# Optimization experiments

Hardware: AMD Instinct MI355X
Metric: run time of the kernel (lower is better)

Reference implementation:

```python
import jax, jax.numpy as jnp
import numpy as np
import math

N = 4096      # nodes
E = 131072    # edges
D = 256       # hidden / out_features
DIN = 16      # distance_map feature dim
H = 2         # attention heads
HD = D // H   # head dim = 128


def setup_inputs() -> dict:
    key = jax.random.key(0)
    ks = jax.random.split(key, 20)
    s = 0.02
    return {
        "input": jax.random.normal(ks[0], (N, D), jnp.float32),
        "adj": jax.random.randint(ks[1], (2, E), 0, N, jnp.int64),
        "h0": jax.random.normal(ks[2], (N, D), jnp.float32),
        "lamda": 1,
        "alpha": jax.random.uniform(ks[3], (1,), jnp.float32),
        "l": 1,
        "distance_map": jax.random.normal(ks[4], (E, DIN), jnp.float32),
        "norm": jax.random.uniform(ks[5], (E,), jnp.float32),
        # GraphConvolution params
        "weight_local": jax.random.normal(ks[6], (2 * D, D), jnp.float32) * s,
        "weight_global": jax.random.normal(ks[7], (2 * D, D), jnp.float32) * s,
        # EA_GCN.lin : Linear(16, D)
        "lin_w": jax.random.normal(ks[8], (D, DIN), jnp.float32) * s,
        "lin_b": jnp.zeros((D,), jnp.float32),
        # EA_GCN.W_EV : 3D -> 2D -> D -> 16 (GELU between)
        "w1": jax.random.normal(ks[9], (2 * D, 3 * D), jnp.float32) * s,
        "b1": jnp.zeros((2 * D,), jnp.float32),
        "w2": jax.random.normal(ks[10], (D, 2 * D), jnp.float32) * s,
        "b2": jnp.zeros((D,), jnp.float32),
        "w3": jax.random.normal(ks[11], (DIN, D), jnp.float32) * s,
        "b3": jnp.zeros((DIN,), jnp.float32),
        # MultiheadAttention params (torch layout: in_proj [3D, D])
        "in_proj_w": jax.random.normal(ks[12], (3 * D, D), jnp.float32) * s,
        "in_proj_b": jnp.zeros((3 * D,), jnp.float32),
        "out_proj_w": jax.random.normal(ks[13], (D, D), jnp.float32) * s,
        "out_proj_b": jnp.zeros((D,), jnp.float32),
    }


def _mha(x, wi, bi, wo, bo):
    # torch MHA, unbatched (N, D) input, eval mode (dropout off)
    qkv = x @ wi.T + bi                      # [N, 3D]
    q, k, v = jnp.split(qkv, 3, axis=-1)
    q = q.reshape(N, H, HD).transpose(1, 0, 2)  # [H, N, HD]
    k = k.reshape(N, H, HD).transpose(1, 0, 2)
    v = v.reshape(N, H, HD).transpose(1, 0, 2)
    scores = jnp.einsum("hnd,hmd->hnm", q, k) / math.sqrt(HD)
    attn = jax.nn.softmax(scores, axis=-1)
    o = jnp.einsum("hnm,hmd->hnd", attn, v)     # [H, N, HD]
    o = o.transpose(1, 0, 2).reshape(N, D)
    return o @ wo.T + bo


def _ea_gcn(x, edge_index, norm, distance_map, lin_w, lin_b, w1, b1, w2, b2, w3, b3):
    src, dst = edge_index[0], edge_index[1]
    edge_attr = distance_map @ lin_w.T + lin_b               # [E, D]
    msg = norm[:, None] * (x[src] + edge_attr)               # gather + combine
    agg = jax.ops.segment_sum(msg, dst, num_segments=N)      # scatter-add
    x_out = agg + x
    h = jnp.concatenate([x_out[src], edge_attr, x_out[dst]], axis=-1)  # [E, 3D]
    h = jax.nn.gelu(h @ w1.T + b1, approximate=False)
    h = jax.nn.gelu(h @ w2.T + b2, approximate=False)
    dm_out = h @ w3.T + b3                                   # [E, 16]
    return x_out, dm_out


def reference(input, adj, h0, lamda, alpha, l, distance_map, norm,
              weight_local, weight_global, lin_w, lin_b,
              w1, b1, w2, b2, w3, b3,
              in_proj_w, in_proj_b, out_proj_w, out_proj_b):
    theta = min(1.0, math.log(lamda / l + 1.0))
    a = alpha[0]
    h_local, dm_out = _ea_gcn(input, adj, norm, distance_map,
                              lin_w, lin_b, w1, b1, w2, b2, w3, b3)
    h_global = _mha(input, in_proj_w, in_proj_b, out_proj_w, out_proj_b)
    support_local = jnp.concatenate([h_local, h0], axis=1)   # [N, 2D]
    r_local = (1.0 - a) * h_local + a * h0
    support_global = jnp.concatenate([h_global, h0], axis=1)
    r_global = (1.0 - a) * h_global + a * h0
    output_local = theta * (support_local @ weight_local) + (1.0 - theta) * r_local
    output_global = theta * (support_global @ weight_global) + (1.0 - theta) * r_global
    output = output_local + output_global                    # residual=False
    return (output, dm_out)
```

## Files before the change

### kernel.cpp

```cpp
#include <hip/hip_runtime.h>
#include <hip/hip_bf16.h>
#include <math.h>

constexpr int N_   = 4096;
constexpr int E_   = 131072;
constexpr int D_   = 256;
constexpr int DIN_ = 16;
constexpr int D3_  = 768;
constexpr int HD_  = 128;

typedef __bf16 bf16_8 __attribute__((ext_vector_type(8)));
typedef float  f32x4  __attribute__((ext_vector_type(4)));
typedef float  f32x4v __attribute__((ext_vector_type(4)));
typedef unsigned int u32x4 __attribute__((ext_vector_type(4)));

__device__ __forceinline__ unsigned short f2b(float f) {
  unsigned int u = __float_as_uint(f);
  u = u + 0x7fffu + ((u >> 16) & 1u);
  return (unsigned short)(u >> 16);
}
__device__ __forceinline__ float b2f(unsigned short s) {
  return __uint_as_float(((unsigned int)s) << 16);
}
__device__ __forceinline__ unsigned int pack2(unsigned short lo, unsigned short hi) {
// ... 444 lines not shown
  for (int m = 0; m < 2; ++m)
#pragma unroll
    for (int n = 0; n < 8; ++n) {
      int col = j0 + n * 16 + r16;
      float bb = opb[col];
#pragma unroll
      for (int rg = 0; rg < 4; ++rg) {
        int row = m0 + wv * 32 + m * 16 + quad * 4 + rg;
        float v = acc[m][n][rg] + bb;
        size_t idx = (size_t)row * D_ + col;
        hgl[idx] = v;
        hgb[idx] = f2b(v);
      }
    }
}

__global__ __launch_bounds__(256) void k_final_mfma(
    const unsigned short* __restrict__ xbp, const unsigned short* __restrict__ h0b,
    const unsigned short* __restrict__ hgb,
    const unsigned short* __restrict__ wlT, const unsigned short* __restrict__ wgT,
    const float* __restrict__ hl, const float* __restrict__ hg, const float* __restrict__ h0,
    const float* __restrict__ alpha_p, const void* lamda_p, const void* l_p,
    float* __restrict__ out) {
  __shared__ unsigned short sA[128][72];
  __shared__ unsigned short sB[128][72];
  const int b   = blockIdx.x;
  const int j0  = (b & 1) * 128;
  const int m0  = (b >> 1) * 128;
  const int tid = threadIdx.x;
  const int lane = tid & 63, wv = tid >> 6;
  const int r16  = lane & 15, quad = lane >> 4;
  const int sr   = tid >> 1, sh = (tid & 1) * 32;

  const f32x4 zz = {0.f, 0.f, 0.f, 0.f};
  f32x4 acc[2][8];
#pragma unroll
  for (int m = 0; m < 2; ++m)
#pragma unroll
    for (int n = 0; n < 8; ++n) acc[m][n] = zz;

  const size_t arow = (size_t)(m0 + sr) * D_;
  const size_t brow = (size_t)(j0 + sr) * 512;

  for (int ki = 0; ki < 16; ++ki) {
    __syncthreads();
    {
      const int gc = ki * 64 + sh;
      const unsigned short* ap =
          (gc < 256) ? xbp + arow + gc
        : (gc < 512) ? h0b + arow + (gc - 256)
        : (gc < 768) ? hgb + arow + (gc - 512)
                     : h0b + arow + (gc - 768);
      const unsigned short* bp = (gc < 512) ? wlT + brow + gc : wgT + brow + (gc - 512);
      const uint4* s    = (const uint4*)ap;
      const uint4* bsrc = (const uint4*)bp;
      uint4* da = (uint4*)&sA[sr][sh];
      uint4* db = (uint4*)&sB[sr][sh];
#pragma unroll
      for (int i = 0; i < 4; ++i) { da[i] = s[i]; db[i] = bsrc[i]; }
    }
    __syncthreads();
#pragma unroll
    for (int kk = 0; kk < 2; ++kk) {
      bf16_8 a0 = frag16(&sA[wv * 32 + r16][kk * 32 + quad * 8]);
      bf16_8 a1 = frag16(&sA[wv * 32 + 16 + r16][kk * 32 + quad * 8]);
#pragma unroll
      for (int n = 0; n < 8; ++n) {
        bf16_8 bf = frag16(&sB[n * 16 + r16][kk * 32 + quad * 8]);
        acc[0][n] = __builtin_amdgcn_mfma_f32_16x16x32_bf16(a0, bf, acc[0][n], 0, 0, 0);
        acc[1][n] = __builtin_amdgcn_mfma_f32_16x16x32_bf16(a1, bf, acc[1][n], 0, 0, 0);
      }
    }
  }
  float theta = fminf(1.f, logf(scalar_as_float(lamda_p) / scalar_as_float(l_p) + 1.f));
  float a = alpha_p[0];
  float omt = 1.f - theta;
#pragma unroll
  for (int m = 0; m < 2; ++m)
#pragma unroll
    for (int n = 0; n < 8; ++n) {
      int col = j0 + n * 16 + r16;
#pragma unroll
      for (int rg = 0; rg < 4; ++rg) {
        int row = m0 + wv * 32 + m * 16 + quad * 4 + rg;
        size_t idx = (size_t)row * D_ + col;
        out[idx] = theta * acc[m][n][rg] +
                   omt * ((1.f - a) * (hl[idx] + hg[idx]) + 2.f * a * h0[idx]);
      }
    }
}

__global__ void k_qk2b(const float* __restrict__ qkv,
                       unsigned short* __restrict__ Qb, unsigned short* __restrict__ Kb) {
  int off = (blockIdx.x * 256 + threadIdx.x) * 8;
  int n = off >> 9, c = off & 511;
  const float* src = qkv + (size_t)n * D3_ + c;
  float4 a = *(const float4*)src;
  float4 b = *(const float4*)(src + 4);
  uint4 p = {pack2(f2b(a.x), f2b(a.y)), pack2(f2b(a.z), f2b(a.w)),
             pack2(f2b(b.x), f2b(b.y)), pack2(f2b(b.z), f2b(b.w))};
  int cc = c & 255;
  int hh = cc >> 7, d = cc & 127;
  unsigned short* dst = (c < 256 ? Qb : Kb) + (size_t)hh * N_ * HD_ + (size_t)n * HD_ + d;
  *(uint4*)dst = p;
}

__global__ __launch_bounds__(256) void k_v2t(const float* __restrict__ qkv,
                                             unsigned short* __restrict__ Vt) {
  __shared__ unsigned short sv[64][136];
  int h = blockIdx.y;
  int n0 = blockIdx.x * 64;
  int tid = threadIdx.x;
#pragma unroll
  for (int it = 0; it < 4; ++it) {
    int off = (tid + it * 256) * 8;
    int r = off >> 7, d = off & 127;
    const float* src = qkv + (size_t)(n0 + r) * D3_ + 2 * D_ + h * HD_ + d;
    float4 a = *(const float4*)src;
    float4 b = *(const float4*)(src + 4);
    uint4 p = {pack2(f2b(a.x), f2b(a.y)), pack2(f2b(a.z), f2b(a.w)),
               pack2(f2b(b.x), f2b(b.y)), pack2(f2b(b.z), f2b(b.w))};
    *(uint4*)&sv[r][d] = p;
  }
  __syncthreads();
#pragma unroll
  for (int it = 0; it < 4; ++it) {
    int off = (tid + it * 256) * 8;
    int d = off >> 6, k = off & 63;
    unsigned short t[8];
#pragma unroll
    for (int j = 0; j < 8; ++j) t[j] = sv[k + j][d];
    uint4 p = {pack2(t[0], t[1]), pack2(t[2], t[3]),
               pack2(t[4], t[5]), pack2(t[6], t[7])};
    *(uint4*)(Vt + (size_t)h * HD_ * N_ + (size_t)d * N_ + n0 + k) = p;
  }
}

__global__ __launch_bounds__(256) void k_attn_mfma(
    const unsigned short* __restrict__ Qb, const unsigned short* __restrict__ Kb,
    const unsigned short* __restrict__ Vt, float* __restrict__ o_out,
    unsigned short* __restrict__ ob) {
  __shared__ unsigned short sK[64][136];
  __shared__ unsigned short sV[128][72];
  __shared__ float          sS[16][68];
  __shared__ unsigned short sP[16][72];
  __shared__ float sm[16], sl[16], sa[16];

  const int tid  = threadIdx.x;
  const int h    = blockIdx.y;
  const int q0   = blockIdx.x * 16;
  const int lane = tid & 63;
  const int wv   = tid >> 6;
  const int r16  = lane & 15;
  const int quad = lane >> 4;

  bf16_8 qf[4];
#pragma unroll
  for (int kk = 0; kk < 4; ++kk)
    qf[kk] = frag16(Qb + (size_t)h * N_ * HD_ + (size_t)(q0 + r16) * HD_ + kk * 32 + quad * 8);

  if (tid < 16) { sm[tid] = -1e30f; sl[tid] = 0.f; }

  const f32x4 zz = {0.f, 0.f, 0.f, 0.f};
  f32x4 o0 = zz, o1 = zz;

  const unsigned short* Kh = Kb + (size_t)h * N_ * HD_;
  const unsigned short* Vh = Vt + (size_t)h * HD_ * N_;

  for (int c0 = 0; c0 < N_; c0 += 64) {
    __syncthreads();
#pragma unroll
    for (int it = 0; it < 4; ++it) {
      int off = (tid + it * 256) * 8;
      int key = off >> 7, d = off & 127;
      *(uint4*)&sK[key][d] = *(const uint4*)(Kh + (size_t)(c0 + key) * HD_ + d);
    }
#pragma unroll
    for (int it = 0; it < 4; ++it) {
      int off = (tid + it * 256) * 8;
      int d = off >> 6, k = off & 63;
      *(uint4*)&sV[d][k] = *(const uint4*)(Vh + (size_t)d * N_ + c0 + k);
    }
    __syncthreads();
    f32x4 s = zz;
#pragma unroll
    for (int kk = 0; kk < 4; ++kk) {
      bf16_8 bf = frag16(&sK[wv * 16 + r16][kk * 32 + quad * 8]);
      s = __builtin_amdgcn_mfma_f32_16x16x32_bf16(qf[kk], bf, s, 0, 0, 0);
    }
    const float sc = 0.08838834764831845f;
#pragma unroll
    for (int r = 0; r < 4; ++r)
      sS[quad * 4 + r][wv * 16 + r16] = s[r] * sc;
    __syncthreads();
    {
      int row = tid >> 4, i = tid & 15;
      float4 v = *(const float4*)&sS[row][i * 4];
      float mx = fmaxf(fmaxf(v.x, v.y), fmaxf(v.z, v.w));
#pragma unroll
      for (int m = 1; m <= 8; m <<= 1) mx = fmaxf(mx, __shfl_xor(mx, m));
      float mo = sm[row];
      float mn = fmaxf(mo, mx);
      float p0 = __expf(v.x - mn), p1 = __expf(v.y - mn);
      float p2 = __expf(v.z - mn), p3 = __expf(v.w - mn);
      float ps = p0 + p1 + p2 + p3;
#pragma unroll
      for (int m = 1; m <= 8; m <<= 1) ps += __shfl_xor(ps, m);
      uint2 pk = {pack2(f2b(p0), f2b(p1)), pack2(f2b(p2), f2b(p3))};
      *(uint2*)&sP[row][i * 4] = pk;
      if (i == 0) {
        float al = __expf(mo - mn);
        sl[row] = sl[row] * al + ps;
        sm[row] = mn;
        sa[row] = al;
      }
    }
    __syncthreads();
    {
      float al0 = sa[quad * 4 + 0], al1 = sa[quad * 4 + 1];
      float al2 = sa[quad * 4 + 2], al3 = sa[quad * 4 + 3];
      o0[0] *= al0; o0[1] *= al1; o0[2] *= al2; o0[3] *= al3;
      o1[0] *= al0; o1[1] *= al1; o1[2] *= al2; o1[3] *= al3;
#pragma unroll
      for (int kk = 0; kk < 2; ++kk) {
        bf16_8 pa = frag16(&sP[r16][kk * 32 + quad * 8]);
        bf16_8 v0 = frag16(&sV[wv * 32 + r16][kk * 32 + quad * 8]);
        bf16_8 v1 = frag16(&sV[wv * 32 + 16 + r16][kk * 32 + quad * 8]);
        o0 = __builtin_amdgcn_mfma_f32_16x16x32_bf16(pa, v0, o0, 0, 0, 0);
        o1 = __builtin_amdgcn_mfma_f32_16x16x32_bf16(pa, v1, o1, 0, 0, 0);
      }
    }
  }
  {
    float i0 = 1.f / sl[quad * 4 + 0], i1 = 1.f / sl[quad * 4 + 1];
    float i2 = 1.f / sl[quad * 4 + 2], i3 = 1.f / sl[quad * 4 + 3];
    float vv[8];
    vv[0] = o0[0] * i0; vv[1] = o0[1] * i1; vv[2] = o0[2] * i2; vv[3] = o0[3] * i3;
    vv[4] = o1[0] * i0; vv[5] = o1[1] * i1; vv[6] = o1[2] * i2; vv[7] = o1[3] * i3;
#pragma unroll
    for (int g = 0; g < 2; ++g)
#pragma unroll
      for (int rg = 0; rg < 4; ++rg) {
        size_t idx = (size_t)(q0 + quad * 4 + rg) * D_ + h * HD_ + wv * 32 + g * 16 + r16;
        float v = vv[g * 4 + rg];
        o_out[idx] = v;
        ob[idx] = f2b(v);
      }
  }
}

__global__ __launch_bounds__(256) void k_final(
    const float* __restrict__ hl, const float* __restrict__ hg, const float* __restrict__ h0,
    const float* __restrict__ Wl, const float* __restrict__ Wg,
    const float* __restrict__ alpha_p, const void* lamda_p, const void* l_p,
    float* __restrict__ out) {
  __shared__ float sA[16][68];
  __shared__ float sB[16][68];
  float theta = fminf(1.f, logf(scalar_as_float(lamda_p) / scalar_as_float(l_p) + 1.f));
  float a = alpha_p[0];
  int bm = blockIdx.y * 64, bn = blockIdx.x * 64;
  int tid = threadIdx.x, tr = tid >> 4, tc = tid & 15;
  float acc[4][4] = {};
  for (int k0 = 0; k0 < 1024; k0 += 16) {
    for (int i = tid; i < 1024; i += 256) {
      int r = i >> 4, c = i & 15;
      int k = k0 + c;
      const float* src = (k < 256) ? hl : (k < 512) ? h0 : (k < 768) ? hg : h0;
      sA[c][r] = src[(size_t)(bm + r) * 256 + (k & 255)];
    }
    for (int i = tid; i < 1024; i += 256) {
      int kk = i >> 6, j = i & 63;
      int k = k0 + kk;
      const float* Bp = (k < 512) ? (Wl + (size_t)k * 256) : (Wg + (size_t)(k - 512) * 256);
      sB[kk][j] = Bp[bn + j];
    }
    __syncthreads();
#pragma unroll
    for (int kk = 0; kk < 16; kk++) {
      float av[4], bv[4];
#pragma unroll
      for (int i = 0; i < 4; i++) av[i] = sA[kk][tr * 4 + i];
#pragma unroll
      for (int j = 0; j < 4; j++) bv[j] = sB[kk][tc * 4 + j];
#pragma unroll
      for (int i = 0; i < 4; i++)
#pragma unroll
        for (int j = 0; j < 4; j++) acc[i][j] += av[i] * bv[j];
    }
    __syncthreads();
  }
  float omt = 1.f - theta;
#pragma unroll
  for (int i = 0; i < 4; i++) {
    int r = bm + tr * 4 + i;
#pragma unroll
    for (int j = 0; j < 4; j++) {
      int c = bn + tc * 4 + j;
      size_t idx = (size_t)r * 256 + c;
      out[idx] = theta * acc[i][j] + omt * ((1.f - a) * (hl[idx] + hg[idx]) + 2.f * a * h0[idx]);
    }
  }
}

__global__ __launch_bounds__(256, 2) void k_mlp_gemm1b(
    const unsigned short* __restrict__ eab, const int* __restrict__ adj,
    const unsigned short* __restrict__ Pac, const unsigned short* __restrict__ wb1,
    const float* __restrict__ b1, unsigned short* __restrict__ t1) {
  __shared__ unsigned short shm[24576];
  unsigned short* lA = shm;
  unsigned short* lB = shm + 8192;
  const int b    = blockIdx.x;
  const int c0   = (b & 1) * 256;
  const int e0   = (b >> 1) * 128;
  const int tid  = threadIdx.x;
  const int lane = tid & 63, wv = tid >> 6;
  const int r16  = lane & 15, quad = lane >> 4;

  const int row0 = e0 + wv * 32 + r16;
  const int row1 = row0 + 16;
  const unsigned short* ea0 = eab + (size_t)row0 * D_ + quad * 8;
  const unsigned short* ea1 = eab + (size_t)row1 * D_ + quad * 8;

  const f32x4 zz = {0.f, 0.f, 0.f, 0.f};
  f32x4 acc[2][16];
#pragma unroll
  for (int m = 0; m < 2; ++m)
#pragma unroll
    for (int n = 0; n < 16; ++n) acc[m][n] = zz;

  for (int ki = 0; ki < 4; ++ki) {
    __syncthreads();
    {
#pragma unroll
      for (int kk = 0; kk < 2; ++kk) {
        gl2lds16(ea0 + ki * 64 + kk * 32, &lA[(wv * 4 + kk) * 512]);
        gl2lds16(ea1 + ki * 64 + kk * 32, &lA[(wv * 4 + 2 + kk) * 512]);
#pragma unroll
        for (int i = 0; i < 4; ++i) {
          int n = wv * 4 + i;
          gl2lds16(wb1 + (size_t)(c0 + n * 16 + r16) * 768 + 256 + ki * 64 + kk * 32 + quad * 8,
                   &lB[(n * 2 + kk) * 512]);
        }
      }
    }
    __builtin_amdgcn_s_waitcnt(0);
    __syncthreads();
#pragma unroll
    for (int kk = 0; kk < 2; ++kk) {
      bf16_8 a0 = frag16(&lA[(wv * 4 + kk) * 512 + lane * 8]);
      bf16_8 a1 = frag16(&lA[(wv * 4 + 2 + kk) * 512 + lane * 8]);
#pragma unroll
      for (int n = 0; n < 16; ++n) {
        bf16_8 bf = frag16(&lB[(n * 2 + kk) * 512 + lane * 8]);
        acc[0][n] = __builtin_amdgcn_mfma_f32_16x16x32_bf16(a0, bf, acc[0][n], 0, 0, 0);
        acc[1][n] = __builtin_amdgcn_mfma_f32_16x16x32_bf16(a1, bf, acc[1][n], 0, 0, 0);
      }
    }
  }
  __syncthreads();
  unsigned short* reg = shm + wv * 4224;
#pragma unroll
  for (int m = 0; m < 2; ++m) {
#pragma unroll
    for (int n = 0; n < 16; ++n)
#pragma unroll
      for (int rg = 0; rg < 4; ++rg)
        reg[(quad * 4 + rg) * 264 + n * 16 + r16] = f2b(acc[m][n][rg]);
#pragma unroll
    for (int it = 0; it < 8; ++it) {
      int flat = it * 64 + lane;
      int row = flat >> 5;
      int g   = flat & 31;
      int er  = e0 + wv * 32 + m * 16 + row;
      int vs  = adj[er];
      int vd  = adj[E_ + er];
      int c   = c0 + g * 8;
      uint4 midq = *(const uint4*)&reg[row * 264 + g * 8];
      uint4 paq  = *(const uint4*)(Pac + (size_t)vs * 1024 + c);
      uint4 pcq  = *(const uint4*)(Pac + (size_t)vd * 1024 + 512 + c);
      float4 ba = *(const float4*)(b1 + c);
      float4 bb = *(const float4*)(b1 + c + 4);
      const unsigned int mv[4] = {midq.x, midq.y, midq.z, midq.w};
      const unsigned int pv[4] = {paq.x, paq.y, paq.z, paq.w};
      const unsigned int cv[4] = {pcq.x, pcq.y, pcq.z, pcq.w};
      const float bl[8] = {ba.x, ba.y, ba.z, ba.w, bb.x, bb.y, bb.z, bb.w};
      unsigned short us[8];
#pragma unroll
      for (int j = 0; j < 8; ++j) {
        unsigned short mw = (j & 1) ? (unsigned short)(mv[j >> 1] >> 16)
                                    : (unsigned short)(mv[j >> 1] & 0xffffu);
        unsigned short pw = (j & 1) ? (unsigned short)(pv[j >> 1] >> 16)
                                    : (unsigned short)(pv[j >> 1] & 0xffffu);
        unsigned short cw = (j & 1) ? (unsigned short)(cv[j >> 1] >> 16)
                                    : (unsigned short)(cv[j >> 1] & 0xffffu);
        float v = b2f(mw) + b2f(pw) + b2f(cw) + bl[j];
        us[j] = f2b(gelu_fast(v));
      }
      uint4 ov = make_uint4(pack2(us[0], us[1]), pack2(us[2], us[3]),
                            pack2(us[4], us[5]), pack2(us[6], us[7]));
      ntstore16(&t1[(size_t)er * 512 + c], ov);
    }
    __syncthreads();
  }
}

__global__ __launch_bounds__(256, 2) void k_mlp_gemm23(
    const unsigned short* __restrict__ t1, const unsigned short* __restrict__ wb2,
    const float* __restrict__ b2, const unsigned short* __restrict__ wb3,
    const float* __restrict__ b3, float* __restrict__ dmo) {
  __shared__ unsigned short shm[24576];
  unsigned short* lA = shm;
  unsigned short* lB = shm + 8192;
  const int e0   = blockIdx.x * 128;
  const int tid  = threadIdx.x;
  const int lane = tid & 63, wv = tid >> 6;
  const int r16  = lane & 15, quad = lane >> 4;

  const int row0 = e0 + wv * 32 + r16;
  const int row1 = row0 + 16;
  const unsigned short* pa0 = t1 + (size_t)row0 * 512 + quad * 8;
  const unsigned short* pa1 = t1 + (size_t)row1 * 512 + quad * 8;

  const f32x4 zz = {0.f, 0.f, 0.f, 0.f};
  f32x4 acc[2][16];
#pragma unroll
  for (int m = 0; m < 2; ++m)
#pragma unroll
    for (int n = 0; n < 16; ++n) acc[m][n] = zz;

  for (int ki = 0; ki < 8; ++ki) {
    __syncthreads();
    {
#pragma unroll
      for (int kk = 0; kk < 2; ++kk) {
        gl2lds16(pa0 + ki * 64 + kk * 32, &lA[(wv * 4 + kk) * 512]);
        gl2lds16(pa1 + ki * 64 + kk * 32, &lA[(wv * 4 + 2 + kk) * 512]);
#pragma unroll
        for (int i = 0; i < 4; ++i) {
          int n = wv * 4 + i;
          gl2lds16(wb2 + (size_t)(n * 16 + r16) * 512 + ki * 64 + kk * 32 + quad * 8,
                   &lB[(n * 2 + kk) * 512]);
        }
      }
    }
    __builtin_amdgcn_s_waitcnt(0);
    __syncthreads();
#pragma unroll
    for (int kk = 0; kk < 2; ++kk) {
      bf16_8 a0 = frag16(&lA[(wv * 4 + kk) * 512 + lane * 8]);
      bf16_8 a1 = frag16(&lA[(wv * 4 + 2 + kk) * 512 + lane * 8]);
#pragma unroll
      for (int n = 0; n < 16; ++n) {
        bf16_8 bf = frag16(&lB[(n * 2 + kk) * 512 + lane * 8]);
        acc[0][n] = __builtin_amdgcn_mfma_f32_16x16x32_bf16(a0, bf, acc[0][n], 0, 0, 0);
        acc[1][n] = __builtin_amdgcn_mfma_f32_16x16x32_bf16(a1, bf, acc[1][n], 0, 0, 0);
      }
    }
  }
  __syncthreads();
  unsigned short* reg = shm + wv * 4224;
  float bb3 = b3[r16];
#pragma unroll
  for (int m = 0; m < 2; ++m) {
#pragma unroll
    for (int n = 0; n < 16; ++n) {
      float bb = b2[n * 16 + r16];
#pragma unroll
      for (int rg = 0; rg < 4; ++rg)
        reg[(quad * 4 + rg) * 264 + n * 16 + r16] = f2b(gelu_fast(acc[m][n][rg] + bb));
    }
    f32x4 acc3 = zz;
#pragma unroll
    for (int ks = 0; ks < 8; ++ks) {
      bf16_8 a = frag16(&reg[r16 * 264 + ks * 32 + quad * 8]);
      bf16_8 b = frag16(wb3 + (size_t)r16 * 256 + ks * 32 + quad * 8);
      acc3 = __builtin_amdgcn_mfma_f32_16x16x32_bf16(a, b, acc3, 0, 0, 0);
    }
#pragma unroll
    for (int rg = 0; rg < 4; ++rg)
      dmo[(size_t)(e0 + wv * 32 + m * 16 + quad * 4 + rg) * DIN_ + r16] = acc3[rg] + bb3;
  }
}

__global__ __launch_bounds__(256, 3) void k_edge_mlp_mfma(
    const float* __restrict__ xout, const int* __restrict__ adj,
    const float* __restrict__ dmap,
    const float* __restrict__ lin_w, const float* __restrict__ lin_b,
    const unsigned short* __restrict__ wb1, const float* __restrict__ b1,
    const unsigned short* __restrict__ wb2, const float* __restrict__ b2,
    const unsigned short* __restrict__ wb3, const float* __restrict__ b3,
    float* __restrict__ dmo) {
  __shared__ unsigned short sLo[8448];
  __shared__ unsigned short sT1[32][520];
  unsigned short (*sA)[136]  = (unsigned short(*)[136])sLo;
  unsigned short (*sT2)[264] = (unsigned short(*)[264])sLo;

  const int tid  = threadIdx.x;
  const int e0   = blockIdx.x * 32;
  const int lane = tid & 63;
  const int wv   = tid >> 6;
  const int r16  = lane & 15;
  const int quad = lane >> 4;

  const int sr = tid >> 3;
  const int t8 = tid & 7;
  const int se = e0 + sr;
  const int vsrc = adj[se];
  const int vdst = adj[E_ + se];

  float4 pf0, pf1, pf2, pf3;
  float4 dm0, dm1, dm2, dm3;
  {
    const float4* sp = (const float4*)(xout + (size_t)vsrc * D_ + t8 * 16);
    pf0 = sp[0]; pf1 = sp[1]; pf2 = sp[2]; pf3 = sp[3];
  }

  const f32x4 zz = {0.f, 0.f, 0.f, 0.f};
  f32x4 acc1[8][2];
#pragma unroll
  for (int i = 0; i < 8; ++i) { acc1[i][0] = zz; acc1[i][1] = zz; }

  for (int c = 0; c < 6; ++c) {
    const int k0 = c * 128;
    __syncthreads();
    {
      unsigned short tmp[16];
      if (c == 2 || c == 3) {
        int jb = (c - 2) * 128 + t8 * 16;
#pragma unroll
        for (int j = 0; j < 16; ++j) {
          const float4* lw = (const float4*)(lin_w + (size_t)(jb + j) * DIN_);
          float4 w0 = lw[0], w1 = lw[1], w2 = lw[2], w3 = lw[3];
          float acc = lin_b[jb + j];
          acc += dm0.x * w0.x + dm0.y * w0.y + dm0.z * w0.z + dm0.w * w0.w;
          acc += dm1.x * w1.x + dm1.y * w1.y + dm1.z * w1.z + dm1.w * w1.w;
          acc += dm2.x * w2.x + dm2.y * w2.y + dm2.z * w2.z + dm2.w * w2.w;
          acc += dm3.x * w3.x + dm3.y * w3.y + dm3.z * w3.z + dm3.w * w3.w;
          tmp[j] = f2b(acc);
        }
      } else {
        tmp[0]  = f2b(pf0.x); tmp[1]  = f2b(pf0.y); tmp[2]  = f2b(pf0.z); tmp[3]  = f2b(pf0.w);
        tmp[4]  = f2b(pf1.x); tmp[5]  = f2b(pf1.y); tmp[6]  = f2b(pf1.z); tmp[7]  = f2b(pf1.w);
        tmp[8]  = f2b(pf2.x); tmp[9]  = f2b(pf2.y); tmp[10] = f2b(pf2.z); tmp[11] = f2b(pf2.w);
        tmp[12] = f2b(pf3.x); tmp[13] = f2b(pf3.y); tmp[14] = f2b(pf3.z); tmp[15] = f2b(pf3.w);
      }
      unsigned short* dstp = &sA[sr][t8 * 16];
      uint4 q0v = {pack2(tmp[0], tmp[1]),   pack2(tmp[2], tmp[3]),
                   pack2(tmp[4], tmp[5]),   pack2(tmp[6], tmp[7])};
      uint4 q1v = {pack2(tmp[8], tmp[9]),   pack2(tmp[10], tmp[11]),
                   pack2(tmp[12], tmp[13]), pack2(tmp[14], tmp[15])};
      *(uint4*)(dstp) = q0v;
      *(uint4*)(dstp + 8) = q1v;
    }
    if (c == 0) {
      const float4* sp = (const float4*)(xout + (size_t)vsrc * D_ + 128 + t8 * 16);
      pf0 = sp[0]; pf1 = sp[1]; pf2 = sp[2]; pf3 = sp[3];
    } else if (c == 1) {
      const float4* dp = (const float4*)(dmap + (size_t)se * DIN_);
      dm0 = ntload4(dp); dm1 = ntload4(dp + 1); dm2 = ntload4(dp + 2); dm3 = ntload4(dp + 3);
    } else if (c == 3) {
      const float4* sp = (const float4*)(xout + (size_t)vdst * D_ + t8 * 16);
      pf0 = sp[0]; pf1 = sp[1]; pf2 = sp[2]; pf3 = sp[3];
    } else if (c == 4) {
      const float4* sp = (const float4*)(xout + (size_t)vdst * D_ + 128 + t8 * 16);
      pf0 = sp[0]; pf1 = sp[1]; pf2 = sp[2]; pf3 = sp[3];
    }
    __syncthreads();
#pragma unroll
    for (int kk = 0; kk < 4; ++kk) {
      bf16_8 a0 = frag16(&sA[r16][kk * 32 + quad * 8]);
      bf16_8 a1 = frag16(&sA[16 + r16][kk * 32 + quad * 8]);
#pragma unroll
      for (int i = 0; i < 8; ++i) {
        const unsigned short* bp =
            wb1 + (size_t)(wv * 128 + i * 16 + r16) * 768 + k0 + kk * 32 + quad * 8;
        bf16_8 bf = frag16(bp);
        acc1[i][0] = __builtin_amdgcn_mfma_f32_16x16x32_bf16(a0, bf, acc1[i][0], 0, 0, 0);
        acc1[i][1] = __builtin_amdgcn_mfma_f32_16x16x32_bf16(a1, bf, acc1[i][1], 0, 0, 0);
      }
    }
  }
#pragma unroll
  for (int i = 0; i < 8; ++i) {
    int col = wv * 128 + i * 16 + r16;
    float bb = b1[col];
#pragma unroll
    for (int r = 0; r < 4; ++r) {
      int row = quad * 4 + r;
      sT1[row][col] = f2b(gelu_exact(acc1[i][0][r] + bb));
      sT1[row + 16][col] = f2b(gelu_exact(acc1[i][1][r] + bb));
    }
  }
  __syncthreads();

  f32x4 acc2[4][2];
#pragma unroll
  for (int i = 0; i < 4; ++i) { acc2[i][0] = zz; acc2[i][1] = zz; }
#pragma unroll 4
  for (int ks = 0; ks < 16; ++ks) {
    bf16_8 a0 = frag16(&sT1[r16][ks * 32 + quad * 8]);
    bf16_8 a1 = frag16(&sT1[16 + r16][ks * 32 + quad * 8]);
#pragma unroll
    for (int i = 0; i < 4; ++i) {
      const unsigned short* bp =
          wb2 + (size_t)(wv * 64 + i * 16 + r16) * 512 + ks * 32 + quad * 8;
      bf16_8 bf = frag16(bp);
      acc2[i][0] = __builtin_amdgcn_mfma_f32_16x16x32_bf16(a0, bf, acc2[i][0], 0, 0, 0);
      acc2[i][1] = __builtin_amdgcn_mfma_f32_16x16x32_bf16(a1, bf, acc2[i][1], 0, 0, 0);
    }
  }
#pragma unroll
  for (int i = 0; i < 4; ++i) {
    int col = wv * 64 + i * 16 + r16;
    float bb = b2[col];
#pragma unroll
    for (int m = 0; m < 2; ++m)
#pragma unroll
      for (int r = 0; r < 4; ++r) {
        int row = m * 16 + quad * 4 + r;
        sT2[row][col] = f2b(gelu_exact(acc2[i][m][r] + bb));
      }
  }
  __syncthreads();

  if (wv < 2) {
    f32x4 acc3 = zz;
#pragma unroll
    for (int ks = 0; ks < 8; ++ks) {
      bf16_8 a = frag16(&sT2[wv * 16 + r16][ks * 32 + quad * 8]);
      bf16_8 b = frag16(wb3 + (size_t)r16 * 256 + ks * 32 + quad * 8);
      acc3 = __builtin_amdgcn_mfma_f32_16x16x32_bf16(a, b, acc3, 0, 0, 0);
    }
    float bb = b3[r16];
#pragma unroll
    for (int r = 0; r < 4; ++r) {
      int row = wv * 16 + quad * 4 + r;
      __builtin_nontemporal_store(acc3[r] + bb, &dmo[(size_t)(e0 + row) * DIN_ + r16]);
    }
  }
}

extern "C" void kernel_launch(void* const* d_in, const int* in_sizes, int n_in,
                              void* d_out, int out_size, void* d_ws, size_t ws_size,
                              hipStream_t stream) {
  const float* input = (const float*)d_in[0];
  const int*   adj   = (const int*)d_in[1];
  const float* h0    = (const float*)d_in[2];
  const void*  lamda = d_in[3];
  const float* alpha = (const float*)d_in[4];
  const void*  lll   = d_in[5];
  const float* dmap  = (const float*)d_in[6];
  const float* nrm   = (const float*)d_in[7];
  const float* Wl    = (const float*)d_in[8];
  const float* Wg    = (const float*)d_in[9];
  const float* lin_w = (const float*)d_in[10];
  const float* lin_b = (const float*)d_in[11];
  const float* w1    = (const float*)d_in[12];
  const float* b1    = (const float*)d_in[13];
  const float* w2    = (const float*)d_in[14];
  const float* b2    = (const float*)d_in[15];
  const float* w3    = (const float*)d_in[16];
  const float* b3    = (const float*)d_in[17];
  const float* ipw   = (const float*)d_in[18];
  const float* ipb   = (const float*)d_in[19];
  const float* opw   = (const float*)d_in[20];
  const float* opb   = (const float*)d_in[21];
  float* out = (float*)d_out;
  float* dmo = out + (size_t)N_ * D_;

  float* ws   = (float*)d_ws;
  float* xout = ws;
  float* qkv  = xout + (size_t)N_ * D_;
  float* atto = qkv  + (size_t)N_ * 3 * D_;
  float* hgl  = atto + (size_t)N_ * D_;
  unsigned short* wb1 = (unsigned short*)(hgl + (size_t)N_ * D_);
  unsigned short* wb2 = wb1 + 512 * 768;
  unsigned short* wb3 = wb2 + 256 * 512;
  unsigned short* Qb  = wb3 + 16 * 256;
  unsigned short* Kb  = Qb + 2 * N_ * HD_;
  unsigned short* Vt  = Kb + 2 * N_ * HD_;
  unsigned short* t1b = Vt + 2 * HD_ * N_;
  unsigned short* t2b = t1b + (size_t)E_ * 512;
  unsigned short* eab = t2b;
  int* cnt  = (int*)(t2b + (size_t)E_ * 256);
  int* off  = cnt + 4096;
  int* cur  = off + 4100;
  int* perm = cur + 4096;
  unsigned short* xbp = (unsigned short*)(perm + E_);
  unsigned short* lwb = xbp + (size_t)N_ * D_;
  unsigned short* inb = lwb + 256 * DIN_;
  unsigned short* h0b = inb + (size_t)N_ * D_;
  unsigned short* hgb = h0b + (size_t)N_ * D_;
  unsigned short* wqb = hgb + (size_t)N_ * D_;
  unsigned short* wlT = wqb + 768 * 256;
  unsigned short* wgT = wlT + 256 * 512;
  unsigned short* opwb = wgT + 256 * 512;
  unsigned short* attob = (unsigned short*)qkv;
  unsigned short* Pac = (unsigned short*)qkv;
  const size_t fast_need = (size_t)((char*)(opwb + 256 * 256) - (char*)d_ws);
  const bool fast = ws_size >= fast_need;

  if (fast) {
    k_prep_w<<<dim3((794624 + 255) / 256), 256, 0, stream>>>(
        w1, w2, w3, lin_w, ipw, opw, wb1, wb2, wb3, lwb, wqb, opwb);
    k_prep_t<<<dim3((262144 + 255) / 256), 256, 0, stream>>>(Wl, Wg, wlT, wgT);
    k_prep_x<<<dim3((2097152 + 255) / 256), 256, 0, stream>>>(input, h0, inb, h0b);

    k_edge_attr_mfma<<<dim3(E_ / 64), 256, 0, stream>>>(dmap, lwb, lin_b, eab);
    k_zero<<<dim3(16), 256, 0, stream>>>(cnt, 4096);
    k_hist<<<dim3(E_ / 256), 256, 0, stream>>>(adj, cnt);
    k_scan<<<dim3(1), 1024, 0, stream>>>(cnt, off, cur);
    k_bucket<<<dim3(E_ / 256), 256, 0, stream>>>(adj, cur, perm);
    k_gather<<<dim3(N_), 256, 0, stream>>>(input, adj, eab, nrm, off, perm, xout);
    k_f2b<<<dim3(N_ * D_ / 256), 256, 0, stream>>>(xout, xbp, N_ * D_);

    k_qkv_mfma<<<dim3(192), 256, 0, stream>>>(inb, wqb, ipb, qkv);
    k_qk2b<<<dim3(N_ * 512 / 8 / 256), 256, 0, stream>>>(qkv, Qb, Kb);
    k_v2t<<<dim3(N_ / 64, 2), 256, 0, stream>>>(qkv, Vt);
    k_attn_mfma<<<dim3(N_ / 16, 2), 256, 0, stream>>>(Qb, Kb, Vt, atto, attob);
    k_outproj_mfma<<<dim3(64), 256, 0, stream>>>(attob, opwb, opb, hgl, hgb);

    k_final_mfma<<<dim3(64), 256, 0, stream>>>(xbp, h0b, hgb, wlT, wgT,
                                               xout, hgl, h0, alpha, lamda, lll, out);

    k_node_pac<<<dim3(256), 256, 0, stream>>>(xbp, wb1, Pac);
    k_mlp_gemm1b<<<dim3(E_ / 128 * 2), 256, 0, stream>>>(eab, adj, Pac, wb1, b1, t1b);
    k_mlp_gemm23<<<dim3(E_ / 128), 256, 0, stream>>>(t1b, wb2, b2, wb3, b3, dmo);
  } else {
    k_f2b<<<dim3((512 * 768 + 255) / 256), 256, 0, stream>>>(w1, wb1, 512 * 768);
    k_f2b<<<dim3((256 * 512 + 255) / 256), 256, 0, stream>>>(w2, wb2, 256 * 512);
    k_f2b<<<dim3((16 * 256 + 255) / 256), 256, 0, stream>>>(w3, wb3, 16 * 256);
    k_copy4<<<dim3(N_ * D_ / 4 / 256), 256, 0, stream>>>((const float4*)input, (float4*)xout,
                                                         N_ * D_ / 4);
    k_scatter<<<dim3(E_ / 4), 256, 0, stream>>>(input, adj, dmap, nrm, lin_w, lin_b, xout);
    k_gemm_bt<<<dim3(D3_ / 64, N_ / 64), 256, 0, stream>>>(input, ipw, ipb, qkv, N_, D3_, D_);
    k_qk2b<<<dim3(N_ * 512 / 8 / 256), 256, 0, stream>>>(qkv, Qb, Kb);
    k_v2t<<<dim3(N_ / 64, 2), 256, 0, stream>>>(qkv, Vt);
    k_attn_mfma<<<dim3(N_ / 16, 2), 256, 0, stream>>>(Qb, Kb, Vt, atto, (unsigned short*)qkv);
    k_gemm_bt<<<dim3(D_ / 64, N_ / 64), 256, 0, stream>>>(atto, opw, opb, hgl, N_, D_, D_);
    k_final<<<dim3(4, N_ / 64), 256, 0, stream>>>(xout, hgl, h0, Wl, Wg, alpha, lamda, lll, out);
    k_edge_mlp_mfma<<<dim3(E_ / 32), 256, 0, stream>>>(xout, adj, dmap, lin_w, lin_b,
                                                       wb1, b1, wb2, b2, wb3, b3, dmo);
  }
}
```

Baseline: 596.1 us.

## Fuse edge MLP layers 1-3 into one kernel, dropping t1 intermediate

```diff
diff --git a/kernel.cpp b/kernel.cpp
--- a/kernel.cpp
+++ b/kernel.cpp
@@ -770,110 +770,10 @@
   }
 }
 
-__global__ __launch_bounds__(256, 2) void k_mlp_gemm1b(
+__global__ __launch_bounds__(256, 1) void k_mlp_f123(
     const unsigned short* __restrict__ eab, const int* __restrict__ adj,
     const unsigned short* __restrict__ Pac, const unsigned short* __restrict__ wb1,
-    const float* __restrict__ b1, unsigned short* __restrict__ t1) {
-  __shared__ unsigned short shm[24576];
-  unsigned short* lA = shm;
-  unsigned short* lB = shm + 8192;
-  const int b    = blockIdx.x;
-  const int c0   = (b & 1) * 256;
-  const int e0   = (b >> 1) * 128;
-  const int tid  = threadIdx.x;
-  const int lane = tid & 63, wv = tid >> 6;
-  const int r16  = lane & 15, quad = lane >> 4;
-
-  const int row0 = e0 + wv * 32 + r16;
-  const int row1 = row0 + 16;
-  const unsigned short* ea0 = eab + (size_t)row0 * D_ + quad * 8;
-  const unsigned short* ea1 = eab + (size_t)row1 * D_ + quad * 8;
-
-  const f32x4 zz = {0.f, 0.f, 0.f, 0.f};
-  f32x4 acc[2][16];
-#pragma unroll
-  for (int m = 0; m < 2; ++m)
-#pragma unroll
-    for (int n = 0; n < 16; ++n) acc[m][n] = zz;
-
-  for (int ki = 0; ki < 4; ++ki) {
-    __syncthreads();
-    {
-#pragma unroll
-      for (int kk = 0; kk < 2; ++kk) {
-        gl2lds16(ea0 + ki * 64 + kk * 32, &lA[(wv * 4 + kk) * 512]);
-        gl2lds16(ea1 + ki * 64 + kk * 32, &lA[(wv * 4 + 2 + kk) * 512]);
-#pragma unroll
-        for (int i = 0; i < 4; ++i) {
-          int n = wv * 4 + i;
-          gl2lds16(wb1 + (size_t)(c0 + n * 16 + r16) * 768 + 256 + ki * 64 + kk * 32 + quad * 8,
-                   &lB[(n * 2 + kk) * 512]);
-        }
-      }
-    }
-    __builtin_amdgcn_s_waitcnt(0);
-    __syncthreads();
-#pragma unroll
-    for (int kk = 0; kk < 2; ++kk) {
-      bf16_8 a0 = frag16(&lA[(wv * 4 + kk) * 512 + lane * 8]);
-      bf16_8 a1 = frag16(&lA[(wv * 4 + 2 + kk) * 512 + lane * 8]);
-#pragma unroll
-      for (int n = 0; n < 16; ++n) {
-        bf16_8 bf = frag16(&lB[(n * 2 + kk) * 512 + lane * 8]);
-        acc[0][n] = __builtin_amdgcn_mfma_f32_16x16x32_bf16(a0, bf, acc[0][n], 0, 0, 0);
-        acc[1][n] = __builtin_amdgcn_mfma_f32_16x16x32_bf16(a1, bf, acc[1][n], 0, 0, 0);
-      }
-    }
-  }
-  __syncthreads();
-  unsigned short* reg = shm + wv * 4224;
-#pragma unroll
-  for (int m = 0; m < 2; ++m) {
-#pragma unroll
-    for (int n = 0; n < 16; ++n)
-#pragma unroll
-      for (int rg = 0; rg < 4; ++rg)
-        reg[(quad * 4 + rg) * 264 + n * 16 + r16] = f2b(acc[m][n][rg]);
-#pragma unroll
-    for (int it = 0; it < 8; ++it) {
-      int flat = it * 64 + lane;
-      int row = flat >> 5;
-      int g   = flat & 31;
-      int er  = e0 + wv * 32 + m * 16 + row;
-      int vs  = adj[er];
-      int vd  = adj[E_ + er];
-      int c   = c0 + g * 8;
-      uint4 midq = *(const uint4*)&reg[row * 264 + g * 8];
-      uint4 paq  = *(const uint4*)(Pac + (size_t)vs * 1024 + c);
-      uint4 pcq  = *(const uint4*)(Pac + (size_t)vd * 1024 + 512 + c);
-      float4 ba = *(const float4*)(b1 + c);
-      float4 bb = *(const float4*)(b1 + c + 4);
-      const unsigned int mv[4] = {midq.x, midq.y, midq.z, midq.w};
-      const unsigned int pv[4] = {paq.x, paq.y, paq.z, paq.w};
-      const unsigned int cv[4] = {pcq.x, pcq.y, pcq.z, pcq.w};
-      const float bl[8] = {ba.x, ba.y, ba.z, ba.w, bb.x, bb.y, bb.z, bb.w};
-      unsigned short us[8];
-#pragma unroll
-      for (int j = 0; j < 8; ++j) {
-        unsigned short mw = (j & 1) ? (unsigned short)(mv[j >> 1] >> 16)
-                                    : (unsigned short)(mv[j >> 1] & 0xffffu);
-        unsigned short pw = (j & 1) ? (unsigned short)(pv[j >> 1] >> 16)
-                                    : (unsigned short)(pv[j >> 1] & 0xffffu);
-        unsigned short cw = (j & 1) ? (unsigned short)(cv[j >> 1] >> 16)
-                                    : (unsigned short)(cv[j >> 1] & 0xffffu);
-        float v = b2f(mw) + b2f(pw) + b2f(cw) + bl[j];
-        us[j] = f2b(gelu_fast(v));
-      }
-      uint4 ov = make_uint4(pack2(us[0], us[1]), pack2(us[2], us[3]),
-                            pack2(us[4], us[5]), pack2(us[6], us[7]));
-      ntstore16(&t1[(size_t)er * 512 + c], ov);
-    }
-    __syncthreads();
-  }
-}
-
-__global__ __launch_bounds__(256, 2) void k_mlp_gemm23(
-    const unsigned short* __restrict__ t1, const unsigned short* __restrict__ wb2,
+    const float* __restrict__ b1, const unsigned short* __restrict__ wb2,
     const float* __restrict__ b2, const unsigned short* __restrict__ wb3,
     const float* __restrict__ b3, float* __restrict__ dmo) {
   __shared__ unsigned short shm[24576];
@@ -886,47 +786,112 @@
 
   const int row0 = e0 + wv * 32 + r16;
   const int row1 = row0 + 16;
-  const unsigned short* pa0 = t1 + (size_t)row0 * 512 + quad * 8;
-  const unsigned short* pa1 = t1 + (size_t)row1 * 512 + quad * 8;
+  const unsigned short* ea0 = eab + (size_t)row0 * D_ + quad * 8;
+  const unsigned short* ea1 = eab + (size_t)row1 * D_ + quad * 8;
 
   const f32x4 zz = {0.f, 0.f, 0.f, 0.f};
-  f32x4 acc[2][16];
+  f32x4 acc2[2][16];
 #pragma unroll
   for (int m = 0; m < 2; ++m)
 #pragma unroll
-    for (int n = 0; n < 16; ++n) acc[m][n] = zz;
-
-  for (int ki = 0; ki < 8; ++ki) {
-    __syncthreads();
-    {
+    for (int n = 0; n < 16; ++n) acc2[m][n] = zz;
+
+  unsigned short* reg = shm + wv * 2176;
+
+  for (int q = 0; q < 4; ++q) {
+    const int cq = q * 128;
+    f32x4 acc1[2][8];
+#pragma unroll
+    for (int m = 0; m < 2; ++m)
+#pragma unroll
+      for (int n = 0; n < 8; ++n) acc1[m][n] = zz;
+
+    for (int ki = 0; ki < 4; ++ki) {
+      __syncthreads();
+      {
+#pragma unroll
+        for (int kk = 0; kk < 2; ++kk) {
+          gl2lds16(ea0 + ki * 64 + kk * 32, &lA[(wv * 4 + kk) * 512]);
+          gl2lds16(ea1 + ki * 64 + kk * 32, &lA[(wv * 4 + 2 + kk) * 512]);
+#pragma unroll
+          for (int i = 0; i < 2; ++i) {
+            int n = wv * 2 + i;
+            gl2lds16(wb1 + (size_t)(cq + n * 16 + r16) * 768 + 256 + ki * 64 + kk * 32 + quad * 8,
+                     &lB[(n * 2 + kk) * 512]);
+          }
+        }
+      }
+      __builtin_amdgcn_s_waitcnt(0);
+      __syncthreads();
 #pragma unroll
       for (int kk = 0; kk < 2; ++kk) {
-        gl2lds16(pa0 + ki * 64 + kk * 32, &lA[(wv * 4 + kk) * 512]);
-        gl2lds16(pa1 + ki * 64 + kk * 32, &lA[(wv * 4 + 2 + kk) * 512]);
-#pragma unroll
-        for (int i = 0; i < 4; ++i) {
-          int n = wv * 4 + i;
-          gl2lds16(wb2 + (size_t)(n * 16 + r16) * 512 + ki * 64 + kk * 32 + quad * 8,
-                   &lB[(n * 2 + kk) * 512]);
+        bf16_8 a0 = frag16(&lA[(wv * 4 + kk) * 512 + lane * 8]);
+        bf16_8 a1 = frag16(&lA[(wv * 4 + 2 + kk) * 512 + lane * 8]);
+#pragma unroll
+        for (int n = 0; n < 8; ++n) {
+          bf16_8 bf = frag16(&lB[(n * 2 + kk) * 512 + lane * 8]);
+          acc1[0][n] = __builtin_amdgcn_mfma_f32_16x16x32_bf16(a0, bf, acc1[0][n], 0, 0, 0);
+          acc1[1][n] = __builtin_amdgcn_mfma_f32_16x16x32_bf16(a1, bf, acc1[1][n], 0, 0, 0);
         }
       }
     }
-    __builtin_amdgcn_s_waitcnt(0);
-    __syncthreads();
-#pragma unroll
-    for (int kk = 0; kk < 2; ++kk) {
-      bf16_8 a0 = frag16(&lA[(wv * 4 + kk) * 512 + lane * 8]);
-      bf16_8 a1 = frag16(&lA[(wv * 4 + 2 + kk) * 512 + lane * 8]);
-#pragma unroll
-      for (int n = 0; n < 16; ++n) {
-        bf16_8 bf = frag16(&lB[(n * 2 + kk) * 512 + lane * 8]);
-        acc[0][n] = __builtin_amdgcn_mfma_f32_16x16x32_bf16(a0, bf, acc[0][n], 0, 0, 0);
-        acc[1][n] = __builtin_amdgcn_mfma_f32_16x16x32_bf16(a1, bf, acc[1][n], 0, 0, 0);
-      }
-    }
-  }
+    __syncthreads();
+
+#pragma unroll
+    for (int m = 0; m < 2; ++m) {
+#pragma unroll
+      for (int n = 0; n < 8; ++n)
+#pragma unroll
+        for (int rg = 0; rg < 4; ++rg)
+          reg[(quad * 4 + rg) * 136 + n * 16 + r16] = f2b(acc1[m][n][rg]);
+#pragma unroll
+      for (int it = 0; it < 4; ++it) {
+        int flat = it * 64 + lane;
+        int row = flat >> 4;
+        int g   = flat & 15;
+        int er  = e0 + wv * 32 + m * 16 + row;
+        int vs  = adj[er];
+        int vd  = adj[E_ + er];
+        int c   = cq + g * 8;
+        uint4 midq = *(const uint4*)&reg[row * 136 + g * 8];
+        uint4 paq  = *(const uint4*)(Pac + (size_t)vs * 1024 + c);
+        uint4 pcq  = *(const uint4*)(Pac + (size_t)vd * 1024 + 512 + c);
+        float4 ba = *(const float4*)(b1 + c);
+        float4 bb = *(const float4*)(b1 + c + 4);
+        const unsigned int mv[4] = {midq.x, midq.y, midq.z, midq.w};
+        const unsigned int pv[4] = {paq.x, paq.y, paq.z, paq.w};
+        const unsigned int cv[4] = {pcq.x, pcq.y, pcq.z, pcq.w};
+        const float bl[8] = {ba.x, ba.y, ba.z, ba.w, bb.x, bb.y, bb.z, bb.w};
+        unsigned short us[8];
+#pragma unroll
+        for (int j = 0; j < 8; ++j) {
+          unsigned short mw = (j & 1) ? (unsigned short)(mv[j >> 1] >> 16)
+                                      : (unsigned short)(mv[j >> 1] & 0xffffu);
+          unsigned short pw = (j & 1) ? (unsigned short)(pv[j >> 1] >> 16)
+                                      : (unsigned short)(pv[j >> 1] & 0xffffu);
+          unsigned short cw = (j & 1) ? (unsigned short)(cv[j >> 1] >> 16)
+                                      : (unsigned short)(cv[j >> 1] & 0xffffu);
+          float v = b2f(mw) + b2f(pw) + b2f(cw) + bl[j];
+          us[j] = f2b(gelu_fast(v));
+        }
+        *(uint4*)&reg[row * 136 + g * 8] = make_uint4(
+            pack2(us[0], us[1]), pack2(us[2], us[3]),
+            pack2(us[4], us[5]), pack2(us[6], us[7]));
+      }
+#pragma unroll
+      for (int ks = 0; ks < 4; ++ks) {
+        bf16_8 a = frag16(&reg[r16 * 136 + ks * 32 + quad * 8]);
+#pragma unroll
+        for (int n = 0; n < 16; ++n) {
+          bf16_8 bf = frag16(wb2 + (size_t)(n * 16 + r16) * 512 + cq + ks * 32 + quad * 8);
+          acc2[m][n] = __builtin_amdgcn_mfma_f32_16x16x32_bf16(a, bf, acc2[m][n], 0, 0, 0);
+        }
+      }
+    }
+  }
+
   __syncthreads();
-  unsigned short* reg = shm + wv * 4224;
+  unsigned short* reg3 = shm + wv * 4224;
   float bb3 = b3[r16];
 #pragma unroll
   for (int m = 0; m < 2; ++m) {
@@ -935,12 +900,12 @@
       float bb = b2[n * 16 + r16];
 #pragma unroll
       for (int rg = 0; rg < 4; ++rg)
-        reg[(quad * 4 + rg) * 264 + n * 16 + r16] = f2b(gelu_fast(acc[m][n][rg] + bb));
+        reg3[(quad * 4 + rg) * 264 + n * 16 + r16] = f2b(gelu_fast(acc2[m][n][rg] + bb));
     }
     f32x4 acc3 = zz;
 #pragma unroll
     for (int ks = 0; ks < 8; ++ks) {
-      bf16_8 a = frag16(&reg[r16 * 264 + ks * 32 + quad * 8]);
+      bf16_8 a = frag16(&reg3[r16 * 264 + ks * 32 + quad * 8]);
       bf16_8 b = frag16(wb3 + (size_t)r16 * 256 + ks * 32 + quad * 8);
       acc3 = __builtin_amdgcn_mfma_f32_16x16x32_bf16(a, b, acc3, 0, 0, 0);
     }
@@ -1192,8 +1157,8 @@
                                                xout, hgl, h0, alpha, lamda, lll, out);
 
     k_node_pac<<<dim3(256), 256, 0, stream>>>(xbp, wb1, Pac);
-    k_mlp_gemm1b<<<dim3(E_ / 128 * 2), 256, 0, stream>>>(eab, adj, Pac, wb1, b1, t1b);
-    k_mlp_gemm23<<<dim3(E_ / 128), 256, 0, stream>>>(t1b, wb2, b2, wb3, b3, dmo);
+    k_mlp_f123<<<dim3(E_ / 128), 256, 0, stream>>>(eab, adj, Pac, wb1, b1,
+                                                   wb2, b2, wb3, b3, dmo);
   } else {
     k_f2b<<<dim3((512 * 768 + 255) / 256), 256, 0, stream>>>(w1, wb1, 512 * 768);
     k_f2b<<<dim3((256 * 512 + 255) / 256), 256, 0, stream>>>(w2, wb2, 256 * 512);
```

Result: slower. 916.3 us (+53.7%).
